# Optimization experiments

Measured on AMD Instinct MI355X. Metric: run time of the kernel, lower is better.

The kernel has to match this reference:

```python
import jax, jax.numpy as jnp
import numpy as np

V, N, H = 4, 4096, 128
EDGE_P = 0.002  # sparsity of generated adjacency


def setup_inputs() -> dict:
    key = jax.random.key(0)
    ks = jax.random.split(key, 12)
    # binary adjacency, zero diagonal (dense_to_sparse treats nonzeros as edges)
    adjs = (jax.random.uniform(ks[0], (V, N, N)) < EDGE_P).astype(jnp.float32)
    idx = jnp.arange(N)
    adjs = adjs.at[:, idx, idx].set(0.0)
    s = 0.05
    return {
        "adjs": adjs,
        "w1": jax.random.normal(ks[1], (V, N, H), jnp.float32) * s,
        "b1": jnp.zeros((V, H), jnp.float32),
        "w2": jax.random.normal(ks[2], (V, H, H), jnp.float32) * s,
        "b2": jnp.zeros((V, H), jnp.float32),
        "wa1": jax.random.normal(ks[3], (H, 64), jnp.float32) * s,
        "ba1": jnp.zeros((64,), jnp.float32),
        "wa2": jax.random.normal(ks[4], (64,), jnp.float32) * s,
        "ba2": jnp.zeros((1,), jnp.float32),
        "wf1": jax.random.normal(ks[5], (V * H, 2 * H), jnp.float32) * s,
        "bf1": jnp.zeros((2 * H,), jnp.float32),
        "wf2": jax.random.normal(ks[6], (2 * H, 128), jnp.float32) * s,
        "bf2": jnp.zeros((128,), jnp.float32),
    }


def _gcn_norm(adjs):
    # GCNConv default: A_hat = A + I, A_norm = D^-1/2 A_hat D^-1/2 (edge weight 1)
    n = adjs.shape[-1]
    idx = jnp.arange(n)
    a_hat = (adjs != 0).astype(adjs.dtype).at[:, idx, idx].set(1.0)
    dinv = jax.lax.rsqrt(a_hat.sum(-1))  # [V,N], deg>=1 due to self loops
    return dinv[:, :, None] * a_hat * dinv[:, None, :]


def reference(adjs, w1, b1, w2, b2, wa1, ba1, wa2, ba2, wf1, bf1, wf2, bf2):
    a_norm = _gcn_norm(adjs)  # [V,N,N]
    # initial features X = I_N, so X @ w1 == w1; dropout is inference no-op
    h1 = jax.nn.relu(jnp.einsum('vij,vjh->vih', a_norm, w1) + b1[:, None, :])
    h2 = jax.nn.relu(
        jnp.einsum('vij,vjh->vih', a_norm, jnp.einsum('vnh,vhk->vnk', h1, w2))
        + b2[:, None, :])  # [V,N,H] per-view embeddings
    # attention fusion
    summaries = h2.mean(axis=1)  # [V,H]
    scores = jnp.tanh(summaries @ wa1 + ba1) @ wa2 + ba2[0]  # [V]
    attn = jax.nn.softmax(scores, axis=0)  # [V]
    weighted = h2 * attn[:, None, None]  # [V,N,H]
    fusion_in = jnp.transpose(weighted, (1, 0, 2)).reshape(weighted.shape[1], -1)  # [N, V*H]
    fused = jax.nn.relu(fusion_in @ wf1 + bf1) @ wf2 + bf2  # [N, fusion_out]
    return fused, attn, h2
```

## Files before the change

kernel.cpp:

```cpp
#include <hip/hip_runtime.h>

#define VV 4
#define NN 4096
#define HH 128
#define CAP 64
#define CH 64
#define GR 32
#define FR 16

typedef __attribute__((ext_vector_type(4))) float fvec4;

__global__ __launch_bounds__(256) void k_build_csr(
    const float* __restrict__ adjs, int* __restrict__ nbr,
    int* __restrict__ cnt, float* __restrict__ dinv)
{
    int wave = threadIdx.x >> 6;
    int lane = threadIdx.x & 63;
    int r = blockIdx.x * 4 + wave;
    const fvec4* row = (const fvec4*)(adjs + (size_t)r * NN);
    int* out = nbr + (size_t)r * CAP;
    unsigned long long lm = (1ull << lane) - 1ull;
    int base = 0;
    #pragma unroll 4
    for (int c = 0; c < NN / 256; ++c) {
        fvec4 x = __builtin_nontemporal_load(&row[c * 64 + lane]);
        int c0 = (x.x != 0.f), c1 = (x.y != 0.f), c2 = (x.z != 0.f), c3 = (x.w != 0.f);
        unsigned long long b0 = __ballot(c0), b1 = __ballot(c1);
        unsigned long long b2 = __ballot(c2), b3 = __ballot(c3);
        int pos = base + __popcll(b0 & lm) + __popcll(b1 & lm)
                       + __popcll(b2 & lm) + __popcll(b3 & lm);
        int e = c * 256 + lane * 4;
        if (c0 && pos < CAP) out[pos] = e;     pos += c0;
        if (c1 && pos < CAP) out[pos] = e + 1; pos += c1;
        if (c2 && pos < CAP) out[pos] = e + 2; pos += c2;
        if (c3 && pos < CAP) out[pos] = e + 3; pos += c3;
        base += __popcll(b0) + __popcll(b1) + __popcll(b2) + __popcll(b3);
    }
    if (lane == 0) {
        cnt[r]  = base < CAP ? base : CAP;
        dinv[r] = rsqrtf((float)(base + 1));
    }
}

__global__ __launch_bounds__(128) void k_spmm(
    const float* __restrict__ feat, const float* __restrict__ bias,
    const int* __restrict__ nbr, const int* __restrict__ cnt,
    const float* __restrict__ dinv, float* __restrict__ out)
{
    int r = blockIdx.x;
    int v = r >> 12;
    int h = threadIdx.x;
    __shared__ int   s_j[CAP];
    __shared__ float s_w[CAP];
    int n = cnt[r];
    float dr = dinv[r];
    if (h < n) {
        int j = nbr[(size_t)r * CAP + h];
        s_j[h] = j;
        s_w[h] = dinv[v * NN + j];
    }
    __syncthreads();
    float acc = dr * feat[(size_t)r * HH + h];
    #pragma unroll 4
    for (int k = 0; k < n; ++k)
        acc += s_w[k] * feat[((size_t)(v * NN + s_j[k])) * HH + h];
    float val = dr * acc + bias[v * HH + h];
    out[(size_t)r * HH + h] = val > 0.f ? val : 0.f;
}

__global__ __launch_bounds__(256) void k_gemm_w2(
    const float* __restrict__ h1, const float* __restrict__ w2,
    float* __restrict__ t)
{
    const int bpv = NN / GR;
    int v = blockIdx.x / bpv;
    int rbase = (blockIdx.x % bpv) * GR;
    __shared__ float s_in[GR][HH];
    const float4* src = (const float4*)(h1 + ((size_t)v * NN + rbase) * HH);
    for (int idx = threadIdx.x; idx < GR * HH / 4; idx += 256)
        ((float4*)s_in)[idx] = src[idx];
    __syncthreads();

    int r0 = (threadIdx.x >> 5) * 4;
    int c0 = (threadIdx.x & 31) * 4;
    const float* wv = w2 + (size_t)v * HH * HH;
    float acc[4][4];
    #pragma unroll
    for (int i = 0; i < 4; ++i)
        #pragma unroll
        for (int j = 0; j < 4; ++j) acc[i][j] = 0.f;

    for (int k = 0; k < HH; k += 4) {
        float4 a[4], w[4];
        #pragma unroll
        for (int i = 0; i < 4; ++i) a[i] = *(const float4*)&s_in[r0 + i][k];
        #pragma unroll
        for (int kk = 0; kk < 4; ++kk) w[kk] = *(const float4*)&wv[(size_t)(k + kk) * HH + c0];
        #pragma unroll
        for (int i = 0; i < 4; ++i) {
            #pragma unroll
            for (int j = 0; j < 4; ++j) {
                acc[i][j] += a[i].x * ((const float*)&w[0])[j];
                acc[i][j] += a[i].y * ((const float*)&w[1])[j];
                acc[i][j] += a[i].z * ((const float*)&w[2])[j];
                acc[i][j] += a[i].w * ((const float*)&w[3])[j];
            }
        }
    }
    float* dst = t + ((size_t)v * NN + rbase) * HH;
    #pragma unroll
    for (int i = 0; i < 4; ++i) {
        float4 o = { acc[i][0], acc[i][1], acc[i][2], acc[i][3] };
        *(float4*)&dst[(size_t)(r0 + i) * HH + c0] = o;
    }
}

__global__ __launch_bounds__(128) void k_colsum(
    const float* __restrict__ h2, float* __restrict__ part)
{
    int v = blockIdx.x / CH;
    int c = blockIdx.x % CH;
    int h = threadIdx.x;
    const int rows = NN / CH;
    const float* src = h2 + ((size_t)v * NN + c * rows) * HH;
    float acc = 0.f;
    #pragma unroll 8
    for (int rr = 0; rr < rows; ++rr) acc += src[rr * HH + h];
    part[(size_t)blockIdx.x * HH + h] = acc;
}

__global__ __launch_bounds__(256) void k_attn(
    const float* __restrict__ part, const float* __restrict__ wa1,
    const float* __restrict__ ba1, const float* __restrict__ wa2,
    const float* __restrict__ ba2, float* __restrict__ attn_out,
    float* __restrict__ attn_ws)
{
    __shared__ float s_sum[VV * HH];
    __shared__ float s_red[256];
    __shared__ float s_score[VV];
    for (int p = threadIdx.x; p < VV * HH; p += 256) {
        int v = p / HH, h = p % HH;
        float a = 0.f;
        for (int c = 0; c < CH; ++c) a += part[(size_t)(v * CH + c) * HH + h];
        s_sum[p] = a * (1.0f / NN);
    }
    __syncthreads();
    int v = threadIdx.x >> 6, u = threadIdx.x & 63;
    float a = ba1[u];
    for (int k = 0; k < HH; ++k) a += s_sum[v * HH + k] * wa1[k * 64 + u];
    s_red[threadIdx.x] = tanhf(a) * wa2[u];
    __syncthreads();
    if (threadIdx.x < VV) {
        float sc = ba2[0];
        for (int uu = 0; uu < 64; ++uu) sc += s_red[threadIdx.x * 64 + uu];
        s_score[threadIdx.x] = sc;
    }
    __syncthreads();
    if (threadIdx.x == 0) {
        float m = s_score[0];
        for (int i = 1; i < VV; ++i) m = fmaxf(m, s_score[i]);
        float e[VV], den = 0.f;
        for (int i = 0; i < VV; ++i) { e[i] = __expf(s_score[i] - m); den += e[i]; }
        for (int i = 0; i < VV; ++i) {
            float av = e[i] / den;
            attn_out[i] = av;
            attn_ws[i]  = av;
        }
    }
}

__global__ __launch_bounds__(256) void k_fusion(
    const float* __restrict__ h2, const float* __restrict__ attn_ws,
    const float* __restrict__ wf1, const float* __restrict__ bf1,
    const float* __restrict__ wf2, const float* __restrict__ bf2,
    float* __restrict__ fused)
{
    __shared__ float s_in[FR][VV * HH];
    __shared__ float s_hid[FR][2 * HH];
    int nbase = blockIdx.x * FR;
    float at[VV];
    #pragma unroll
    for (int v = 0; v < VV; ++v) at[v] = attn_ws[v];

    for (int idx = threadIdx.x; idx < FR * VV * HH / 4; idx += 256) {
        int r  = idx >> 7;
        int c4 = idx & 127;
        int v  = c4 >> 5;
        int h4 = c4 & 31;
        const float4* srcr = (const float4*)(h2 + ((size_t)v * NN + nbase + r) * HH);
        float4 x = srcr[h4];
        float s = at[v];
        x.x *= s; x.y *= s; x.z *= s; x.w *= s;
        ((float4*)&s_in[r][0])[c4] = x;
    }
    __syncthreads();

    {
        int r0 = (threadIdx.x >> 6) * 4;
        int c0 = (threadIdx.x & 63) * 4;
        float acc[4][4];
        #pragma unroll
        for (int i = 0; i < 4; ++i)
            #pragma unroll
            for (int j = 0; j < 4; ++j) acc[i][j] = 0.f;
        for (int k = 0; k < VV * HH; k += 4) {
            float4 a[4], w[4];
            #pragma unroll
            for (int i = 0; i < 4; ++i) a[i] = *(const float4*)&s_in[r0 + i][k];
            #pragma unroll
            for (int kk = 0; kk < 4; ++kk)
                w[kk] = *(const float4*)&wf1[(size_t)(k + kk) * (2 * HH) + c0];
            #pragma unroll
            for (int i = 0; i < 4; ++i)
                #pragma unroll
                for (int j = 0; j < 4; ++j) {
                    acc[i][j] += a[i].x * ((const float*)&w[0])[j];
                    acc[i][j] += a[i].y * ((const float*)&w[1])[j];
                    acc[i][j] += a[i].z * ((const float*)&w[2])[j];
                    acc[i][j] += a[i].w * ((const float*)&w[3])[j];
                }
        }
        #pragma unroll
        for (int j = 0; j < 4; ++j) {
            float b = bf1[c0 + j];
            #pragma unroll
            for (int i = 0; i < 4; ++i) {
                float hv = acc[i][j] + b;
                s_hid[r0 + i][c0 + j] = hv > 0.f ? hv : 0.f;
            }
        }
    }
    __syncthreads();

    {
        int r0 = (threadIdx.x >> 5) * 2;
        int c0 = (threadIdx.x & 31) * 4;
        float acc[2][4];
        #pragma unroll
        for (int i = 0; i < 2; ++i)
            #pragma unroll
            for (int j = 0; j < 4; ++j) acc[i][j] = 0.f;
        for (int k = 0; k < 2 * HH; k += 4) {
            float4 a[2], w[4];
            #pragma unroll
            for (int i = 0; i < 2; ++i) a[i] = *(const float4*)&s_hid[r0 + i][k];
            #pragma unroll
            for (int kk = 0; kk < 4; ++kk)
                w[kk] = *(const float4*)&wf2[(size_t)(k + kk) * HH + c0];
            #pragma unroll
            for (int i = 0; i < 2; ++i)
                #pragma unroll
                for (int j = 0; j < 4; ++j) {
                    acc[i][j] += a[i].x * ((const float*)&w[0])[j];
                    acc[i][j] += a[i].y * ((const float*)&w[1])[j];
                    acc[i][j] += a[i].z * ((const float*)&w[2])[j];
                    acc[i][j] += a[i].w * ((const float*)&w[3])[j];
                }
        }
        #pragma unroll
        for (int i = 0; i < 2; ++i) {
            float4 o;
            o.x = acc[i][0] + bf2[c0 + 0];
            o.y = acc[i][1] + bf2[c0 + 1];
            o.z = acc[i][2] + bf2[c0 + 2];
            o.w = acc[i][3] + bf2[c0 + 3];
            *(float4*)&fused[(size_t)(nbase + r0 + i) * HH + c0] = o;
        }
    }
}

extern "C" void kernel_launch(void* const* d_in, const int* in_sizes, int n_in,
                              void* d_out, int out_size, void* d_ws, size_t ws_size,
                              hipStream_t stream)
{
    const float* adjs = (const float*)d_in[0];
    const float* w1   = (const float*)d_in[1];
    const float* b1   = (const float*)d_in[2];
    const float* w2   = (const float*)d_in[3];
    const float* b2   = (const float*)d_in[4];
    const float* wa1  = (const float*)d_in[5];
    const float* ba1  = (const float*)d_in[6];
    const float* wa2  = (const float*)d_in[7];
    const float* ba2  = (const float*)d_in[8];
    const float* wf1  = (const float*)d_in[9];
    const float* bf1  = (const float*)d_in[10];
    const float* wf2  = (const float*)d_in[11];
    const float* bf2  = (const float*)d_in[12];

    float* out   = (float*)d_out;
    float* fused = out;
    float* attn  = out + (size_t)NN * HH;
    float* h2    = attn + VV;

    char* w = (char*)d_ws;
    int*   nbr    = (int*)w;    w += (size_t)VV * NN * CAP * sizeof(int);
    int*   cnt    = (int*)w;    w += (size_t)VV * NN * sizeof(int);
    float* dinv   = (float*)w;  w += (size_t)VV * NN * sizeof(float);
    float* h1     = (float*)w;  w += (size_t)VV * NN * HH * sizeof(float);
    float* t      = (float*)w;  w += (size_t)VV * NN * HH * sizeof(float);
    float* part   = (float*)w;  w += (size_t)VV * CH * HH * sizeof(float);
    float* attnws = (float*)w;  w += (size_t)VV * sizeof(float);

    k_build_csr<<<VV * NN / 4, 256, 0, stream>>>(adjs, nbr, cnt, dinv);
    k_spmm<<<VV * NN, 128, 0, stream>>>(w1, b1, nbr, cnt, dinv, h1);
    k_gemm_w2<<<VV * NN / GR, 256, 0, stream>>>(h1, w2, t);
    k_spmm<<<VV * NN, 128, 0, stream>>>(t, b2, nbr, cnt, dinv, h2);
    k_colsum<<<VV * CH, 128, 0, stream>>>(h2, part);
    k_attn<<<1, 256, 0, stream>>>(part, wa1, ba1, wa2, ba2, attn, attnws);
    k_fusion<<<NN / FR, 256, 0, stream>>>(h2, attnws, wf1, bf1, wf2, bf2, fused);
}
```

Before: 153.8 us.

## Fuse layer-2 SpMM, W2 GEMM, bias/ReLU and column sums via reassociation

Layer 2 is reassociated as (A·h1)·W2 instead of A·(h1·W2). The aggregation, the W2 GEMM, bias, ReLU and the per-block column partial sums now run in one kernel, which removes the intermediate t buffer and the separate colsum launch. The first SpMM handles four rows per 512-thread block, and the fusion and attention kernels move to 512 threads. The trade-off is a k_attn single block that now reduces 256 partials per view instead of 64, and the reassociation changes floating-point rounding order.

Result: no change. 154.9 us (+0.7%).

```diff
diff --git a/kernel.cpp b/kernel.cpp
--- a/kernel.cpp
+++ b/kernel.cpp
@@ -4,9 +4,9 @@
 #define NN 4096
 #define HH 128
 #define CAP 64
-#define CH 64
-#define GR 32
+#define R2 16
 #define FR 16
+#define CHP (NN / R2)
 
 typedef __attribute__((ext_vector_type(4))) float fvec4;
 
@@ -42,62 +42,103 @@
     }
 }
 
-__global__ __launch_bounds__(128) void k_spmm(
-    const float* __restrict__ feat, const float* __restrict__ bias,
+__global__ __launch_bounds__(512) void k_spmm1(
+    const float* __restrict__ w1, const float* __restrict__ b1,
     const int* __restrict__ nbr, const int* __restrict__ cnt,
-    const float* __restrict__ dinv, float* __restrict__ out)
-{
-    int r = blockIdx.x;
+    const float* __restrict__ dinv, float* __restrict__ h1)
+{
+    int g = threadIdx.x >> 7;
+    int h = threadIdx.x & 127;
+    int r = blockIdx.x * 4 + g;
     int v = r >> 12;
-    int h = threadIdx.x;
-    __shared__ int   s_j[CAP];
-    __shared__ float s_w[CAP];
+    __shared__ int   s_j[4][CAP];
+    __shared__ float s_w[4][CAP];
     int n = cnt[r];
     float dr = dinv[r];
     if (h < n) {
         int j = nbr[(size_t)r * CAP + h];
-        s_j[h] = j;
-        s_w[h] = dinv[v * NN + j];
-    }
-    __syncthreads();
-    float acc = dr * feat[(size_t)r * HH + h];
+        s_j[g][h] = j;
+        s_w[g][h] = dinv[v * NN + j];
+    }
+    __syncthreads();
+    float acc = dr * w1[(size_t)r * HH + h];
     #pragma unroll 4
     for (int k = 0; k < n; ++k)
-        acc += s_w[k] * feat[((size_t)(v * NN + s_j[k])) * HH + h];
-    float val = dr * acc + bias[v * HH + h];
-    out[(size_t)r * HH + h] = val > 0.f ? val : 0.f;
-}
-
-__global__ __launch_bounds__(256) void k_gemm_w2(
+        acc += s_w[g][k] * w1[((size_t)(v * NN + s_j[g][k])) * HH + h];
+    float val = dr * acc + b1[v * HH + h];
+    h1[(size_t)r * HH + h] = val > 0.f ? val : 0.f;
+}
+
+__global__ __launch_bounds__(256) void k_layer2(
     const float* __restrict__ h1, const float* __restrict__ w2,
-    float* __restrict__ t)
-{
-    const int bpv = NN / GR;
+    const float* __restrict__ b2, const int* __restrict__ nbr,
+    const int* __restrict__ cnt, const float* __restrict__ dinv,
+    float* __restrict__ h2, float* __restrict__ part)
+{
+    const int bpv = NN / R2;
     int v = blockIdx.x / bpv;
-    int rbase = (blockIdx.x % bpv) * GR;
-    __shared__ float s_in[GR][HH];
-    const float4* src = (const float4*)(h1 + ((size_t)v * NN + rbase) * HH);
-    for (int idx = threadIdx.x; idx < GR * HH / 4; idx += 256)
-        ((float4*)s_in)[idx] = src[idx];
-    __syncthreads();
-
-    int r0 = (threadIdx.x >> 5) * 4;
+    int gr0 = blockIdx.x * R2;
+    __shared__ int   s_n[R2];
+    __shared__ float s_dr[R2];
+    __shared__ int   s_j[R2][CAP];
+    __shared__ float s_w[R2][CAP];
+    __shared__ float s_u[R2][HH];
+    __shared__ float s_p[8][HH];
+
+    if (threadIdx.x < R2) {
+        s_n[threadIdx.x]  = cnt[gr0 + threadIdx.x];
+        s_dr[threadIdx.x] = dinv[gr0 + threadIdx.x];
+    }
+    __syncthreads();
+    for (int idx = threadIdx.x; idx < R2 * CAP; idx += 256) {
+        int rr = idx >> 6, kk = idx & 63;
+        if (kk < s_n[rr]) {
+            int j = nbr[(size_t)(gr0 + rr) * CAP + kk];
+            s_j[rr][kk] = j;
+            s_w[rr][kk] = dinv[v * NN + j];
+        }
+    }
+    __syncthreads();
+
+    {
+        int rr  = threadIdx.x >> 4;
+        int t16 = threadIdx.x & 15;
+        int h0  = t16 * 8;
+        int n   = s_n[rr];
+        float dr = s_dr[rr];
+        const float* self = h1 + (size_t)(gr0 + rr) * HH + h0;
+        float a[8];
+        #pragma unroll
+        for (int q = 0; q < 8; ++q) a[q] = dr * self[q];
+        #pragma unroll 2
+        for (int k = 0; k < n; ++k) {
+            float wj = s_w[rr][k];
+            const float4* src = (const float4*)(h1 + ((size_t)(v * NN + s_j[rr][k])) * HH + h0);
+            float4 x0 = src[0], x1 = src[1];
+            a[0] += wj * x0.x; a[1] += wj * x0.y; a[2] += wj * x0.z; a[3] += wj * x0.w;
+            a[4] += wj * x1.x; a[5] += wj * x1.y; a[6] += wj * x1.z; a[7] += wj * x1.w;
+        }
+        #pragma unroll
+        for (int q = 0; q < 8; ++q) s_u[rr][h0 + q] = dr * a[q];
+    }
+    __syncthreads();
+
+    int r0 = (threadIdx.x >> 5) * 2;
     int c0 = (threadIdx.x & 31) * 4;
     const float* wv = w2 + (size_t)v * HH * HH;
-    float acc[4][4];
+    float acc[2][4];
     #pragma unroll
-    for (int i = 0; i < 4; ++i)
+    for (int i = 0; i < 2; ++i)
         #pragma unroll
         for (int j = 0; j < 4; ++j) acc[i][j] = 0.f;
-
     for (int k = 0; k < HH; k += 4) {
-        float4 a[4], w[4];
-        #pragma unroll
-        for (int i = 0; i < 4; ++i) a[i] = *(const float4*)&s_in[r0 + i][k];
+        float4 a[2], w[4];
+        #pragma unroll
+        for (int i = 0; i < 2; ++i) a[i] = *(const float4*)&s_u[r0 + i][k];
         #pragma unroll
         for (int kk = 0; kk < 4; ++kk) w[kk] = *(const float4*)&wv[(size_t)(k + kk) * HH + c0];
         #pragma unroll
-        for (int i = 0; i < 4; ++i) {
+        for (int i = 0; i < 2; ++i)
             #pragma unroll
             for (int j = 0; j < 4; ++j) {
                 acc[i][j] += a[i].x * ((const float*)&w[0])[j];
@@ -105,31 +146,33 @@
                 acc[i][j] += a[i].z * ((const float*)&w[2])[j];
                 acc[i][j] += a[i].w * ((const float*)&w[3])[j];
             }
-        }
-    }
-    float* dst = t + ((size_t)v * NN + rbase) * HH;
+    }
+    float p[4];
     #pragma unroll
-    for (int i = 0; i < 4; ++i) {
+    for (int j = 0; j < 4; ++j) {
+        float b = b2[v * HH + c0 + j];
+        float v0 = acc[0][j] + b, v1 = acc[1][j] + b;
+        v0 = v0 > 0.f ? v0 : 0.f;
+        v1 = v1 > 0.f ? v1 : 0.f;
+        acc[0][j] = v0; acc[1][j] = v1;
+        p[j] = v0 + v1;
+    }
+    #pragma unroll
+    for (int i = 0; i < 2; ++i) {
         float4 o = { acc[i][0], acc[i][1], acc[i][2], acc[i][3] };
-        *(float4*)&dst[(size_t)(r0 + i) * HH + c0] = o;
-    }
-}
-
-__global__ __launch_bounds__(128) void k_colsum(
-    const float* __restrict__ h2, float* __restrict__ part)
-{
-    int v = blockIdx.x / CH;
-    int c = blockIdx.x % CH;
-    int h = threadIdx.x;
-    const int rows = NN / CH;
-    const float* src = h2 + ((size_t)v * NN + c * rows) * HH;
-    float acc = 0.f;
-    #pragma unroll 8
-    for (int rr = 0; rr < rows; ++rr) acc += src[rr * HH + h];
-    part[(size_t)blockIdx.x * HH + h] = acc;
-}
-
-__global__ __launch_bounds__(256) void k_attn(
+        *(float4*)&h2[(size_t)(gr0 + r0 + i) * HH + c0] = o;
+    }
+    *(float4*)&s_p[threadIdx.x >> 5][c0] = *(float4*)p;
+    __syncthreads();
+    if (threadIdx.x < HH) {
+        float a = 0.f;
+        #pragma unroll
+        for (int q = 0; q < 8; ++q) a += s_p[q][threadIdx.x];
+        part[(size_t)blockIdx.x * HH + threadIdx.x] = a;
+    }
+}
+
+__global__ __launch_bounds__(512) void k_attn(
     const float* __restrict__ part, const float* __restrict__ wa1,
     const float* __restrict__ ba1, const float* __restrict__ wa2,
     const float* __restrict__ ba2, float* __restrict__ attn_out,
@@ -138,17 +181,20 @@
     __shared__ float s_sum[VV * HH];
     __shared__ float s_red[256];
     __shared__ float s_score[VV];
-    for (int p = threadIdx.x; p < VV * HH; p += 256) {
-        int v = p / HH, h = p % HH;
+    {
+        int v = threadIdx.x >> 7, h = threadIdx.x & 127;
         float a = 0.f;
-        for (int c = 0; c < CH; ++c) a += part[(size_t)(v * CH + c) * HH + h];
-        s_sum[p] = a * (1.0f / NN);
-    }
-    __syncthreads();
-    int v = threadIdx.x >> 6, u = threadIdx.x & 63;
-    float a = ba1[u];
-    for (int k = 0; k < HH; ++k) a += s_sum[v * HH + k] * wa1[k * 64 + u];
-    s_red[threadIdx.x] = tanhf(a) * wa2[u];
+        #pragma unroll 8
+        for (int c = 0; c < CHP; ++c) a += part[(size_t)(v * CHP + c) * HH + h];
+        s_sum[v * HH + h] = a * (1.0f / NN);
+    }
+    __syncthreads();
+    if (threadIdx.x < 256) {
+        int v = threadIdx.x >> 6, u = threadIdx.x & 63;
+        float a = ba1[u];
+        for (int k = 0; k < HH; ++k) a += s_sum[v * HH + k] * wa1[k * 64 + u];
+        s_red[threadIdx.x] = tanhf(a) * wa2[u];
+    }
     __syncthreads();
     if (threadIdx.x < VV) {
         float sc = ba2[0];
@@ -169,7 +215,7 @@
     }
 }
 
-__global__ __launch_bounds__(256) void k_fusion(
+__global__ __launch_bounds__(512) void k_fusion(
     const float* __restrict__ h2, const float* __restrict__ attn_ws,
     const float* __restrict__ wf1, const float* __restrict__ bf1,
     const float* __restrict__ wf2, const float* __restrict__ bf2,
@@ -182,7 +228,7 @@
     #pragma unroll
     for (int v = 0; v < VV; ++v) at[v] = attn_ws[v];
 
-    for (int idx = threadIdx.x; idx < FR * VV * HH / 4; idx += 256) {
+    for (int idx = threadIdx.x; idx < FR * VV * HH / 4; idx += 512) {
         int r  = idx >> 7;
         int c4 = idx & 127;
         int v  = c4 >> 5;
@@ -196,57 +242,20 @@
     __syncthreads();
 
     {
-        int r0 = (threadIdx.x >> 6) * 4;
+        int r0 = (threadIdx.x >> 6) * 2;
         int c0 = (threadIdx.x & 63) * 4;
-        float acc[4][4];
-        #pragma unroll
-        for (int i = 0; i < 4; ++i)
+        float acc[2][4];
+        #pragma unroll
+        for (int i = 0; i < 2; ++i)
             #pragma unroll
             for (int j = 0; j < 4; ++j) acc[i][j] = 0.f;
         for (int k = 0; k < VV * HH; k += 4) {
-            float4 a[4], w[4];
-            #pragma unroll
-            for (int i = 0; i < 4; ++i) a[i] = *(const float4*)&s_in[r0 + i][k];
+            float4 a[2], w[4];
+            #pragma unroll
+            for (int i = 0; i < 2; ++i) a[i] = *(const float4*)&s_in[r0 + i][k];
             #pragma unroll
             for (int kk = 0; kk < 4; ++kk)
                 w[kk] = *(const float4*)&wf1[(size_t)(k + kk) * (2 * HH) + c0];
-            #pragma unroll
-            for (int i = 0; i < 4; ++i)
-                #pragma unroll
-                for (int j = 0; j < 4; ++j) {
-                    acc[i][j] += a[i].x * ((const float*)&w[0])[j];
-                    acc[i][j] += a[i].y * ((const float*)&w[1])[j];
-                    acc[i][j] += a[i].z * ((const float*)&w[2])[j];
-                    acc[i][j] += a[i].w * ((const float*)&w[3])[j];
-                }
-        }
-        #pragma unroll
-        for (int j = 0; j < 4; ++j) {
-            float b = bf1[c0 + j];
-            #pragma unroll
-            for (int i = 0; i < 4; ++i) {
-                float hv = acc[i][j] + b;
-                s_hid[r0 + i][c0 + j] = hv > 0.f ? hv : 0.f;
-            }
-        }
-    }
-    __syncthreads();
-
-    {
-        int r0 = (threadIdx.x >> 5) * 2;
-        int c0 = (threadIdx.x & 31) * 4;
-        float acc[2][4];
-        #pragma unroll
-        for (int i = 0; i < 2; ++i)
-            #pragma unroll
-            for (int j = 0; j < 4; ++j) acc[i][j] = 0.f;
-        for (int k = 0; k < 2 * HH; k += 4) {
-            float4 a[2], w[4];
-            #pragma unroll
-            for (int i = 0; i < 2; ++i) a[i] = *(const float4*)&s_hid[r0 + i][k];
-            #pragma unroll
-            for (int kk = 0; kk < 4; ++kk)
-                w[kk] = *(const float4*)&wf2[(size_t)(k + kk) * HH + c0];
             #pragma unroll
             for (int i = 0; i < 2; ++i)
                 #pragma unroll
@@ -258,14 +267,43 @@
                 }
         }
         #pragma unroll
-        for (int i = 0; i < 2; ++i) {
-            float4 o;
-            o.x = acc[i][0] + bf2[c0 + 0];
-            o.y = acc[i][1] + bf2[c0 + 1];
-            o.z = acc[i][2] + bf2[c0 + 2];
-            o.w = acc[i][3] + bf2[c0 + 3];
-            *(float4*)&fused[(size_t)(nbase + r0 + i) * HH + c0] = o;
-        }
+        for (int j = 0; j < 4; ++j) {
+            float b = bf1[c0 + j];
+            #pragma unroll
+            for (int i = 0; i < 2; ++i) {
+                float hv = acc[i][j] + b;
+                s_hid[r0 + i][c0 + j] = hv > 0.f ? hv : 0.f;
+            }
+        }
+    }
+    __syncthreads();
+
+    {
+        int r0 = threadIdx.x >> 5;
+        int c0 = (threadIdx.x & 31) * 4;
+        float acc[4];
+        #pragma unroll
+        for (int j = 0; j < 4; ++j) acc[j] = 0.f;
+        for (int k = 0; k < 2 * HH; k += 4) {
+            float4 a = *(const float4*)&s_hid[r0][k];
+            float4 w[4];
+            #pragma unroll
+            for (int kk = 0; kk < 4; ++kk)
+                w[kk] = *(const float4*)&wf2[(size_t)(k + kk) * HH + c0];
+            #pragma unroll
+            for (int j = 0; j < 4; ++j) {
+                acc[j] += a.x * ((const float*)&w[0])[j];
+                acc[j] += a.y * ((const float*)&w[1])[j];
+                acc[j] += a.z * ((const float*)&w[2])[j];
+                acc[j] += a.w * ((const float*)&w[3])[j];
+            }
+        }
+        float4 o;
+        o.x = acc[0] + bf2[c0 + 0];
+        o.y = acc[1] + bf2[c0 + 1];
+        o.z = acc[2] + bf2[c0 + 2];
+        o.w = acc[3] + bf2[c0 + 3];
+        *(float4*)&fused[(size_t)(nbase + r0) * HH + c0] = o;
     }
 }
 
@@ -297,15 +335,12 @@
     int*   cnt    = (int*)w;    w += (size_t)VV * NN * sizeof(int);
     float* dinv   = (float*)w;  w += (size_t)VV * NN * sizeof(float);
     float* h1     = (float*)w;  w += (size_t)VV * NN * HH * sizeof(float);
-    float* t      = (float*)w;  w += (size_t)VV * NN * HH * sizeof(float);
-    float* part   = (float*)w;  w += (size_t)VV * CH * HH * sizeof(float);
+    float* part   = (float*)w;  w += (size_t)VV * CHP * HH * sizeof(float);
     float* attnws = (float*)w;  w += (size_t)VV * sizeof(float);
 
     k_build_csr<<<VV * NN / 4, 256, 0, stream>>>(adjs, nbr, cnt, dinv);
-    k_spmm<<<VV * NN, 128, 0, stream>>>(w1, b1, nbr, cnt, dinv, h1);
-    k_gemm_w2<<<VV * NN / GR, 256, 0, stream>>>(h1, w2, t);
-    k_spmm<<<VV * NN, 128, 0, stream>>>(t, b2, nbr, cnt, dinv, h2);
-    k_colsum<<<VV * CH, 128, 0, stream>>>(h2, part);
-    k_attn<<<1, 256, 0, stream>>>(part, wa1, ba1, wa2, ba2, attn, attnws);
-    k_fusion<<<NN / FR, 256, 0, stream>>>(h2, attnws, wf1, bf1, wf2, bf2, fused);
-}
+    k_spmm1<<<VV * NN / 4, 512, 0, stream>>>(w1, b1, nbr, cnt, dinv, h1);
+    k_layer2<<<VV * NN / R2, 256, 0, stream>>>(h1, w2, b2, nbr, cnt, dinv, h2, part);
+    k_attn<<<1, 512, 0, stream>>>(part, wa1, ba1, wa2, ba2, attn, attnws);
+    k_fusion<<<NN / FR, 512, 0, stream>>>(h2, attnws, wf1, bf1, wf2, bf2, fused);
+}
```
